# Kernel tuning notes

Measured on AMD Instinct MI355X. Metric: run time of the kernel, lower is better.

The kernel has to match this reference:

```python
import jax, jax.numpy as jnp
import numpy as np

N = 3072
F_IN = 512
H1 = 256
HFC = 64
OUT_DIM = 16
NUM_POOL = 3
P_CUT = 30.0  # ps[0]: percentile threshold on positive attention entries
CC_ITERS = 16  # min-label propagation w/ pointer jumping; reach >= 2^16 hops


def l2norm(x):
    # torch F.normalize(p=2, dim=1)
    return x / jnp.clip(jnp.linalg.norm(x, axis=1, keepdims=True), 1e-12, None)


def gcn(x, adj, W, b):
    # standard Kipf GraphConvolution: adj @ (x @ W) + b
    return adj @ (x @ W) + b


def normalize_adj(adj, k):
    n = adj.shape[0]
    A = adj + k * jnp.eye(n, dtype=adj.dtype)
    D = jnp.sqrt(A.sum(0))
    return A / (D[:, None] * D[None, :])


def edge_score(x, adj, a, W, b):
    h = x @ W + b                               # (n, HFC)
    s1 = h @ a[:HFC]                            # (n,)
    s2 = h @ a[HFC:]
    e = jax.nn.sigmoid(s1[:, None] + s2[None, :])
    att = jnp.where(adj > 0, e, jnp.zeros((), e.dtype))
    att = 0.5 * (att + att.T)
    i = jnp.arange(att.shape[0])
    return att.at[i, i].set(1.0)


def percentile_pos(att, p):
    # np.percentile(att[att>0], p) with linear interpolation, jit-safe
    pos = att > 0
    n_pos = pos.sum()
    s = jnp.sort(jnp.where(pos, att, jnp.inf).ravel())
    idx = (n_pos - 1).astype(att.dtype) * (p / 100.0)
    lo = jnp.floor(idx).astype(jnp.int32)
    hi = jnp.ceil(idx).astype(jnp.int32)
    frac = idx - lo.astype(att.dtype)
    return s[lo] * (1.0 - frac) + s[hi] * frac


def cc_labels(mask):
    # connected components via min-label propagation + pointer jumping.
    # diag of mask is always True (att diag = 1), so every node has a neighbor.
    n = mask.shape[0]
    def step(labels, _):
        neigh = jnp.min(jnp.where(mask, labels[None, :], n), axis=1)
        new = jnp.minimum(labels, neigh)
        new = new[new]  # pointer jumping doubles reach each iter
        return new, None
    labels, _ = jax.lax.scan(step, jnp.arange(n, dtype=jnp.int32), None, length=CC_ITERS)
    return labels


def pool(x, adj, att, p):
    cut = percentile_pos(att, p)
    att = att * (att >= cut).astype(att.dtype)
    labels = jax.lax.stop_gradient(cc_labels(att > 0))
    # fixed-shape membership: cluster id = representative (min) node index, padded to N
    C = jax.nn.one_hot(labels, att.shape[0], dtype=x.dtype).T  # (n_clusters=n, n)
    a2 = C @ adj @ C.T
    a2 = 0.5 * (a2 + a2.T)
    cnt = (att > 0).sum(1).astype(x.dtype)  # >=1 since diag survives the cut
    x2 = C @ ((att / cnt[:, None]) @ x)
    return x2, a2, C


def forward(x, adjC, adj, encW0, encb0, encW, encb, fcW, fcb, aW, decW, decb, decW_out, decb_out):
    adjs = [adj]
    adjCs = [adjC]
    xs, Cs, atts = [], [], []
    # ----- encode -----
    for k in range(NUM_POOL):
        x1 = x
        W, b = (encW0, encb0) if k == 0 else (encW[k - 1], encb[k - 1])
        h = jax.nn.relu(gcn(x, adjCs[-1], W, b))
        x = l2norm(h) if k == 0 else l2norm(h + x1)  # residual added for layer idx > 0
        xs.append(x)
        att = edge_score(x, adjs[-1], aW[k], fcW[k], fcb[k])
        x, adjk, C = pool(x, adjs[-1], att, P_CUT)
        adjCk = normalize_adj(adjk, 1.0)  # pool's adjC output is discarded in the original
        x = l2norm(x)
        adjs.append(adjk)
        adjCs.append(adjCk)
        atts.append(att)
        Cs.append(C)
    x = l2norm(jax.nn.elu(gcn(x, adjCs[-1], encW[NUM_POOL - 1], encb[NUM_POOL - 1])))
    xs.append(x)
    # ----- decode -----
    for k in range(NUM_POOL):
        lev = NUM_POOL - k - 1
        x = Cs[lev].T @ x                       # unpool; C is already binary
        x = jnp.concatenate([x, xs[lev]], axis=1)
        x = l2norm(jax.nn.elu(gcn(x, adjCs[lev], decW[k], decb[k])))
    x = gcn(x, adjCs[0], decW_out, decb_out)
    logp = jax.nn.log_softmax(x, axis=1)
    return logp, jnp.stack(Cs), jnp.stack(atts)


def setup_inputs() -> dict:
    key = jax.random.key(0)
    ks = jax.random.split(key, 12)
    x = jax.random.normal(ks[0], (N, F_IN), jnp.float32)
    u = jax.random.uniform(ks[1], (N, N))
    m = (u < 16.0 / N).astype(jnp.float32)  # avg degree ~16
    adj = jnp.maximum(m, m.T)
    i = jnp.arange(N)
    adj = adj.at[i, i].set(1.0)
    adjC = normalize_adj(adj, 1.0)

    def xav(k, shape):
        fan_in = shape[-2] if len(shape) > 1 else shape[-1]
        return jax.random.normal(k, shape, jnp.float32) * (1.0 / np.sqrt(fan_in))

    return {
        "x": x, "adjC": adjC, "adj": adj,
        "encW0": xav(ks[2], (F_IN, H1)), "encb0": jnp.zeros((H1,), jnp.float32),
        "encW": xav(ks[3], (NUM_POOL, H1, H1)), "encb": jnp.zeros((NUM_POOL, H1), jnp.float32),
        "fcW": xav(ks[4], (NUM_POOL, H1, HFC)), "fcb": jnp.zeros((NUM_POOL, HFC), jnp.float32),
        "aW": xav(ks[5], (NUM_POOL, 2 * HFC)),
        "decW": xav(ks[6], (NUM_POOL, 2 * H1, H1)), "decb": jnp.zeros((NUM_POOL, H1), jnp.float32),
        "decW_out": xav(ks[7], (H1, OUT_DIM)), "decb_out": jnp.zeros((OUT_DIM,), jnp.float32),
    }


def reference(x, adjC, adj, encW0, encb0, encW, encb, fcW, fcb, aW, decW, decb, decW_out, decb_out):
    return forward(x, adjC, adj, encW0, encb0, encW, encb, fcW, fcb, aW, decW, decb, decW_out, decb_out)
```

## Files before the change

### kernel.cpp

```cpp
#include <hip/hip_runtime.h>
#include <math.h>

#define NN 3072
#define FF 256
#define CAPE (1<<18)
#define MAXCH 3200

struct Scal {
  int nnzS, nnz2, nzero, mtot, ncht;
  int lo, hi, rank_rem, below_acc, c_le;
  unsigned prefix, vlo, minabove;
  float frac, cut;
};

__device__ __forceinline__ float sigm(float x){ return 1.0f/(1.0f+expf(-x)); }

__global__ __launch_bounds__(256) void k_count_dense(const float* __restrict__ A, int* __restrict__ rowcnt, float* __restrict__ Drow){
  int i=blockIdx.x, t=threadIdx.x;
  int c=0; float sm=0.f;
  for(int j=t;j<NN;j+=256){ float a=A[(size_t)i*NN+j]; if(a!=0.0f||j==i) c++; sm+=a; }
  __shared__ int s[256]; __shared__ float fs[256];
  s[t]=c; fs[t]=sm; __syncthreads();
  for(int o=128;o;o>>=1){ if(t<o){ s[t]+=s[t+o]; fs[t]+=fs[t+o]; } __syncthreads(); }
  if(t==0){ rowcnt[i]=s[0]; if(Drow) Drow[i]=sqrtf(fs[0]+1.0f); }
}

__global__ __launch_bounds__(1024) void k_scan(const int* __restrict__ cnt, int* __restrict__ rp, int* __restrict__ total){
  int t=threadIdx.x;
  int a0=cnt[t*3+0], a1=cnt[t*3+1], a2=cnt[t*3+2];
  int loc=a0+a1+a2;
  __shared__ int s[1024];
  s[t]=loc; __syncthreads();
  for(int o=1;o<1024;o<<=1){ int v=(t>=o)?s[t-o]:0; __syncthreads(); s[t]+=v; __syncthreads(); }
  int excl=s[t]-loc;
  rp[t*3+0]=excl; rp[t*3+1]=excl+a0; rp[t*3+2]=excl+a0+a1;
  if(t==1023){ rp[NN]=s[t]; *total=s[t]; }
}

__global__ __launch_bounds__(256) void k_fill_dense(const float* __restrict__ A, const float* __restrict__ ACd, const float* __restrict__ D,
    const int* __restrict__ rp, int* __restrict__ rows, int* __restrict__ cols, float* __restrict__ aval, float* __restrict__ acval){
  int i=blockIdx.x, t=threadIdx.x;
  const int CH=NN/256;
  int j0=t*CH; int c=0;
  for(int u=0;u<CH;u++){ int j=j0+u; float a=A[(size_t)i*NN+j]; if(a!=0.0f||j==i) c++; }
  __shared__ int s[256]; s[t]=c; __syncthreads();
  for(int o=1;o<256;o<<=1){ int v=(t>=o)?s[t-o]:0; __syncthreads(); s[t]+=v; __syncthreads(); }
  int pos=rp[i]+s[t]-c;
  float Di = D?D[i]:0.0f;
  for(int u=0;u<CH;u++){ int j=j0+u; float a=A[(size_t)i*NN+j];
    if(a!=0.0f||j==i){
      if(pos<CAPE){
        rows[pos]=i; cols[pos]=j; aval[pos]=a;
        acval[pos]= ACd? ACd[(size_t)i*NN+j] : (a+(j==i?1.0f:0.0f))/(Di*D[j]);
      }
      pos++;
    }
  }
}

__global__ __launch_bounds__(256) void k_gemm(const float* __restrict__ A, const float* __restrict__ B, float* __restrict__ C,
                                              int M, int K, int Nc){
  __shared__ float As[16][68];
  __shared__ float Bs[16][68];
  int tid=threadIdx.x;
  int tx=tid&15, ty=tid>>4;
  int bm=blockIdx.y*64, bn=blockIdx.x*64;
  int lm=tid>>2, lk=(tid&3)*4;
  int kr=tid>>4, nf=(tid&15)*4;
  float acc[4][4]={};
  for(int k0=0;k0<K;k0+=16){
    float4 a4=*(const float4*)(A+(size_t)(bm+lm)*K+k0+lk);
    As[lk+0][lm]=a4.x; As[lk+1][lm]=a4.y; As[lk+2][lm]=a4.z; As[lk+3][lm]=a4.w;
    float4 b4=*(const float4*)(B+(size_t)(k0+kr)*Nc+bn+nf);
    *(float4*)&Bs[kr][nf]=b4;
    __syncthreads();
#pragma unroll
    for(int kk=0;kk<16;kk++){
      float4 av=*(const float4*)&As[kk][ty*4];
      float4 bv=*(const float4*)&Bs[kk][tx*4];
      float am[4]={av.x,av.y,av.z,av.w};
      float bb[4]={bv.x,bv.y,bv.z,bv.w};
#pragma unroll
      for(int i2=0;i2<4;i2++)
#pragma unroll
        for(int j2=0;j2<4;j2++) acc[i2][j2]+=am[i2]*bb[j2];
    }
    __syncthreads();
  }
  for(int i2=0;i2<4;i2++){
    float4 o=make_float4(acc[i2][0],acc[i2][1],acc[i2][2],acc[i2][3]);
    *(float4*)(C+(size_t)(bm+ty*4+i2)*Nc+bn+tx*4)=o;
  }
}

__global__ __launch_bounds__(256) void k_gemm16(const float* __restrict__ X, const float* __restrict__ W, float* __restrict__ T){
  int idx=blockIdx.x*256+threadIdx.x;
  if(idx>=NN*16) return;
  int i=idx>>4, o=idx&15;
  float s=0.f;
  for(int kk=0;kk<FF;kk++) s+=X[(size_t)i*FF+kk]*W[kk*16+o];
  T[idx]=s;
}

__global__ __launch_bounds__(256) void k_spmm_gcn(const int* __restrict__ rp, const int* __restrict__ cols, const float* __restrict__ vals,
    const float* __restrict__ X, const float* __restrict__ bias, const float* __restrict__ resid, float* __restrict__ out, int act){
  int wid=blockIdx.x*4+(threadIdx.x>>6);
  int lane=threadIdx.x&63;
  if(wid>=NN) return;
  int e0=rp[wid], e1=rp[wid+1];
  float4 acc=make_float4(0,0,0,0);
  for(int e=e0;e<e1;e++){
    float v=vals[e]; int c=cols[e];
    float4 xv=*(const float4*)(X+(size_t)c*FF+lane*4);
    acc.x+=v*xv.x; acc.y+=v*xv.y; acc.z+=v*xv.z; acc.w+=v*xv.w;
  }
  float4 bv=*(const float4*)(bias+lane*4);
  acc.x+=bv.x; acc.y+=bv.y; acc.z+=bv.z; acc.w+=bv.w;
  if(act==0){
    acc.x=fmaxf(acc.x,0.f); acc.y=fmaxf(acc.y,0.f); acc.z=fmaxf(acc.z,0.f); acc.w=fmaxf(acc.w,0.f);
  } else {
    acc.x=acc.x>0.f?acc.x:expm1f(acc.x); acc.y=acc.y>0.f?acc.y:expm1f(acc.y);
    acc.z=acc.z>0.f?acc.z:expm1f(acc.z); acc.w=acc.w>0.f?acc.w:expm1f(acc.w);
  }
  if(resid){
    float4 r=*(const float4*)(resid+(size_t)wid*FF+lane*4);
    acc.x+=r.x; acc.y+=r.y; acc.z+=r.z; acc.w+=r.w;
  }
  float ss=acc.x*acc.x+acc.y*acc.y+acc.z*acc.z+acc.w*acc.w;
  for(int o=32;o;o>>=1) ss+=__shfl_xor(ss,o);
  float nrm=fmaxf(sqrtf(ss),1e-12f);
  float4 o4=make_float4(acc.x/nrm,acc.y/nrm,acc.z/nrm,acc.w/nrm);
  *(float4*)(out+(size_t)wid*FF+lane*4)=o4;
}

__global__ __launch_bounds__(256) void k_spmm_plain(const int* __restrict__ rp, const int* __restrict__ cols, const float* __restrict__ vals,
    const float* __restrict__ X, float* __restrict__ out){
  int wid=blockIdx.x*4+(threadIdx.x>>6);
  int lane=threadIdx.x&63;
  if(wid>=NN) return;
  int e0=rp[wid], e1=rp[wid+1];
  float4 acc=make_float4(0,0,0,0);
  for(int e=e0;e<e1;e++){
    if(e>=CAPE) break;
    float v=vals[e]; int c=cols[e];
    float4 xv=*(const float4*)(X+(size_t)c*FF+lane*4);
    acc.x+=v*xv.x; acc.y+=v*xv.y; acc.z+=v*xv.z; acc.w+=v*xv.w;
  }
  *(float4*)(out+(size_t)wid*FF+lane*4)=acc;
}

__global__ __launch_bounds__(64) void k_edge(const float* __restrict__ X, const float* __restrict__ fw, const float* __restrict__ fb,
    const float* __restrict__ av, float* __restrict__ s1, float* __restrict__ s2, Scal* sc){
  int i=blockIdx.x, l=threadIdx.x;
  if(i==0&&l==0) sc->nzero=0;
  __shared__ float xr[FF];
  *(float4*)&xr[l*4]=*(const float4*)(X+(size_t)i*FF+l*4);
  __syncthreads();
  float h=fb[l];
  for(int kk=0;kk<FF;kk++) h+=xr[kk]*fw[kk*64+l];
  float p1=h*av[l], p2=h*av[64+l];
  for(int o=32;o;o>>=1){ p1+=__shfl_xor(p1,o); p2+=__shfl_xor(p2,o); }
  if(l==0){ s1[i]=p1; s2[i]=p2; }
}

__global__ __launch_bounds__(256) void k_att_row(const int* __restrict__ rp, const int* __restrict__ cols,
    const float* __restrict__ s1, const float* __restrict__ s2, float* __restrict__ attD, float* __restrict__ cand, Scal* sc){
  __shared__ float row[NN];
  __shared__ int wred[4];
  int i=blockIdx.x, t=threadIdx.x;
  for(int j=t;j<NN;j+=256) row[j]=0.f;
  __syncthreads();
  int e0=rp[i], e1=rp[i+1];
  float s1i=s1[i], s2i=s2[i];
  int nz=0;
  for(int e=e0+t;e<e1;e+=256){
    int j=cols[e];
    float v=(j==i)?1.0f:0.5f*(sigm(s1i+s2[j])+sigm(s1[j]+s2i));
    row[j]=v;
    if(e<CAPE) cand[e]=v;
    if(!(v>0.f)) nz++;
  }
  for(int o=32;o;o>>=1) nz+=__shfl_xor(nz,o);
  if((t&63)==0) wred[t>>6]=nz;
  __syncthreads();
  if(t==0){ int s=wred[0]+wred[1]+wred[2]+wred[3]; if(s) atomicAdd(&sc->nzero,s); }
  float* orow=attD+(size_t)i*NN;
  for(int j=t*4;j<NN;j+=1024) *(float4*)(orow+j)=*(const float4*)&row[j];
}

__global__ void k_prep(Scal* sc){
  int np=sc->nnzS - sc->nzero;
  float idx=(float)(np-1)*(30.0f/100.0f);
  float fl=floorf(idx), ce=ceilf(idx);
  sc->lo=(int)fl; sc->hi=(int)ce; sc->frac=idx-fl;
  sc->rank_rem=sc->lo;
  sc->below_acc=0;
  sc->minabove=0xFFFFFFFFu;
}

template<int PHASE>
__global__ __launch_bounds__(256) void k_hist(const float* __restrict__ cand, const Scal* __restrict__ sc, unsigned* __restrict__ bins){
  const int NB = (PHASE==0)?16384:256;
  __shared__ unsigned h[NB];
  int t=threadIdx.x;
  for(int b=t;b<NB;b+=256) h[b]=0;
  __syncthreads();
  int n=sc->nnzS; if(n>CAPE) n=CAPE;
  unsigned pref=sc->prefix;
  int stride=gridDim.x*256;
  for(int e=blockIdx.x*256+t; e<n; e+=stride){
    float v=cand[e];
    if(!(v>0.f)) continue;
    unsigned bb=__float_as_uint(v);
    if(PHASE==0) atomicAdd(&h[bb>>16],1u);
    else if(PHASE==1){ if((bb>>16)==pref) atomicAdd(&h[(bb>>8)&0xFFu],1u); }
    else { if((bb>>8)==pref) atomicAdd(&h[bb&0xFFu],1u); }
  }
  __syncthreads();
  for(int b=t;b<NB;b+=256){ unsigned c=h[b]; if(c) atomicAdd(&bins[b],c); }
}

template<int PHASE>
__global__ __launch_bounds__(256) void k_pick(const unsigned* __restrict__ bins, Scal* sc){
  const int NB=(PHASE==0)?16384:256;
  const int PER=NB/256;
  __shared__ int part[256];
  __shared__ int selbin; __shared__ int below_sel;
  int t=threadIdx.x;
  int b0=t*PER;
  int sum=0;
  for(int u=0;u<PER;u++) sum+=(int)bins[b0+u];
  part[t]=sum; __syncthreads();
  for(int o=1;o<256;o<<=1){ int v=(t>=o)?part[t-o]:0; __syncthreads(); part[t]+=v; __syncthreads(); }
  int incl=part[t], excl=incl-sum;
  int r=sc->rank_rem;
  if(r>=excl && r<incl){
    int run=excl;
    for(int u=0;u<PER;u++){
      int c=(int)bins[b0+u];
      if(r<run+c){ selbin=b0+u; below_sel=run; break; }
      run+=c;
    }
  }
  __syncthreads();
  if(t==0){
    sc->rank_rem=r-below_sel;
    sc->below_acc+=below_sel;
    if(PHASE==0) sc->prefix=(unsigned)selbin;
    else if(PHASE==1) sc->prefix=(sc->prefix<<8)|(unsigned)selbin;
    else{
      sc->vlo=(sc->prefix<<8)|(unsigned)selbin;
      sc->c_le=sc->below_acc+(int)bins[selbin];
    }
  }
}

__global__ __launch_bounds__(256) void k_minabove(const float* __restrict__ cand, Scal* sc){
  int n=sc->nnzS; if(n>CAPE) n=CAPE;
  unsigned vlo=sc->vlo;
  int tid=threadIdx.x, lane=tid&63;
  int stride=gridDim.x*256;
  for(int base=blockIdx.x*256; base<n; base+=stride){
    int e=base+tid;
    unsigned b=0xFFFFFFFFu;
    if(e<n){ float v=cand[e]; if(v>0.f){ unsigned bb=__float_as_uint(v); if(bb>vlo) b=bb; } }
    for(int o=32;o;o>>=1){ unsigned ob=__shfl_xor(b,o); b=ob<b?ob:b; }
    if(lane==0&&b!=0xFFFFFFFFu) atomicMin(&sc->minabove,b);
  }
}

__global__ void k_cut(Scal* sc){
  float slo=__uint_as_float(sc->vlo);
  float shi;
  if(sc->hi==sc->lo) shi=slo;
  else if(sc->c_le>sc->hi) shi=slo;
  else shi=__uint_as_float(sc->minabove);
  sc->cut=slo*(1.0f-sc->frac)+shi*sc->frac;
}

__global__ __launch_bounds__(256) void k_pc_count(const int* __restrict__ rp, const float* __restrict__ cand, const Scal* __restrict__ sc,
    int* __restrict__ rowcnt, float* __restrict__ cntf){
  int wid=blockIdx.x*4+(threadIdx.x>>6);
  int lane=threadIdx.x&63;
  if(wid>=NN) return;
  int e0=rp[wid], e1=rp[wid+1];
  float cut=sc->cut;
  int c=0;
  for(int e=e0+lane;e<e1;e+=64){ if(e<CAPE && cand[e]>=cut) c++; }
  for(int o=32;o;o>>=1) c+=__shfl_xor(c,o);
  if(lane==0){ rowcnt[wid]=c; cntf[wid]=(float)c; }
}

__global__ __launch_bounds__(256) void k_pc_fill(const int* __restrict__ rp, const int* __restrict__ cols, const float* __restrict__ cand,
    const Scal* __restrict__ sc, const int* __restrict__ rp2, int* __restrict__ rows2, int* __restrict__ cols2, float* __restrict__ pval,
    const float* __restrict__ cntf){
  int wid=blockIdx.x*4+(threadIdx.x>>6);
  int lane=threadIdx.x&63;
  if(wid>=NN) return;
  int e0=rp[wid], e1=rp[wid+1];
  float cut=sc->cut, cf=cntf[wid];
  int base=rp2[wid];
  for(int eb=e0;eb<e1;eb+=64){
    int e=eb+lane;
    bool p=(e<e1)&&(e<CAPE)&&(cand[e]>=cut);
    unsigned long long m=__ballot(p);
    if(p){
      int pos=base+__popcll(m&((1ull<<lane)-1ull));
      if(pos<CAPE){ rows2[pos]=wid; cols2[pos]=cols[e]; pval[pos]=cand[e]/cf; }
    }
    base+=__popcll(m);
  }
}

__global__ __launch_bounds__(1024) void k_cc(const int* __restrict__ rows2, const int* __restrict__ cols2, Scal* sc,
    int* __restrict__ labk, int* __restrict__ moff_g, int* __restrict__ memb,
    int* __restrict__ choff_g, int* __restrict__ chm0_g, int* __restrict__ chm1_g){
  __shared__ int lab[NN];
  __shared__ int cnt[NN];
  __shared__ int mof[NN];
  __shared__ int s[1024];
  __shared__ int chg;
  int t=threadIdx.x;
  for(int i=t;i<NN;i+=1024){ lab[i]=i; cnt[i]=0; }
  int n2=sc->nnz2; if(n2>CAPE) n2=CAPE;
  __syncthreads();
  for(int it=0;it<16;it++){
    if(t==0) chg=0;
    __syncthreads();
    for(int e=t;e<n2;e+=1024){
      int i=rows2[e], j=cols2[e];
      if(i!=j){
        int li=lab[i], lj=lab[j];
        if(lj<li){ if(atomicMin(&lab[i],lj)>lj) chg=1; }
        else if(li<lj){ if(atomicMin(&lab[j],li)>li) chg=1; }
      }
    }
    __syncthreads();
    int l0=lab[t], l1=lab[t+1024], l2=lab[t+2048];
    int v0=lab[l0], v1=lab[l1], v2=lab[l2];
    __syncthreads();
    if(v0<l0){ lab[t]=v0; chg=1; }
    if(v1<l1){ lab[t+1024]=v1; chg=1; }
    if(v2<l2){ lab[t+2048]=v2; chg=1; }
    __syncthreads();
    if(!chg) break;
    __syncthreads();
  }
  for(int i=t;i<NN;i+=1024){ int l=lab[i]; labk[i]=l; atomicAdd(&cnt[l],1); }
  __syncthreads();
  int a0=cnt[t*3+0], a1=cnt[t*3+1], a2=cnt[t*3+2];
  int loc=a0+a1+a2;
  s[t]=loc; __syncthreads();
  for(int o=1;o<1024;o<<=1){ int v=(t>=o)?s[t-o]:0; __syncthreads(); s[t]+=v; __syncthreads(); }
  int excl=s[t]-loc;
  __syncthreads();
  mof[t*3+0]=excl; mof[t*3+1]=excl+a0; mof[t*3+2]=excl+a0+a1;
  cnt[t*3+0]=excl; cnt[t*3+1]=excl+a0; cnt[t*3+2]=excl+a0+a1;
  moff_g[t*3+0]=excl; moff_g[t*3+1]=excl+a0; moff_g[t*3+2]=excl+a0+a1;
  if(t==1023) moff_g[NN]=s[t];
  __syncthreads();
  int ch0=(a0+63)>>6, ch1=(a1+63)>>6, ch2=(a2+63)>>6;
  int locc=ch0+ch1+ch2;
  s[t]=locc; __syncthreads();
  for(int o=1;o<1024;o<<=1){ int v=(t>=o)?s[t-o]:0; __syncthreads(); s[t]+=v; __syncthreads(); }
  int cexcl=s[t]-locc;
  choff_g[t*3+0]=cexcl; choff_g[t*3+1]=cexcl+ch0; choff_g[t*3+2]=cexcl+ch0+ch1;
  if(t==1023){ choff_g[NN]=s[t]; sc->ncht=s[t]; }
  {
    int bases[3]={cexcl,cexcl+ch0,cexcl+ch0+ch1};
    int cnts[3]={a0,a1,a2};
    int nqs[3]={ch0,ch1,ch2};
    for(int u=0;u<3;u++){
      int m0=mof[t*3+u];
      int me=m0+cnts[u];
      for(int q=0;q<nqs[u];q++){
        int idx=bases[u]+q;
        if(idx<MAXCH){
          chm0_g[idx]=m0+q*64;
          int e2=m0+q*64+64; chm1_g[idx]=e2<me?e2:me;
        }
      }
    }
  }
  __syncthreads();
  int lane=t&63, wv=t>>6;
  for(int b=0;b<3;b++){
    int j=b*1024+t;
    int myl=lab[j];
    int rank_w=0,total=0;
#pragma unroll
    for(int l=0;l<64;l++){
      int lb=__shfl(myl,l);
      if(lb==myl){ total++; if(l<lane) rank_w++; }
    }
    for(int w=0;w<16;w++){
      if(wv==w){
        int base=cnt[myl];
        memb[base+rank_w]=j;
        if(rank_w==0) cnt[myl]=base+total;
      }
      __syncthreads();
    }
  }
}

__global__ __launch_bounds__(256) void k_a2e(const int* __restrict__ rowsA, const int* __restrict__ colsA_, const float* __restrict__ aval,
    const Scal* __restrict__ sc, const int* __restrict__ labk, float* __restrict__ dense){
  int e=blockIdx.x*256+threadIdx.x;
  int n=sc->nnzS; if(n>CAPE) n=CAPE;
  int lane=threadIdx.x&63;
  bool valid=(e<n);
  float a=valid?aval[e]:0.f;
  valid=valid&&(a!=0.f);
  int key=0;
  if(valid) key=labk[rowsA[e]]*NN+labk[colsA_[e]];
  unsigned long long act=__ballot(valid);
  while(act){
    int leader=__ffsll(act)-1;
    int lkey=__shfl(key,leader);
    bool same=valid&&(key==lkey);
    float contrib=same?a:0.f;
    for(int o=32;o;o>>=1) contrib+=__shfl_xor(contrib,o);
    if(lane==leader) atomicAdd(&dense[(size_t)lkey],contrib);
    act&=~__ballot(same);
  }
}

__global__ __launch_bounds__(256) void k_x2p(const float* __restrict__ y, const int* __restrict__ memb,
    const int* __restrict__ chm0, const int* __restrict__ chm1, const Scal* __restrict__ sc, float* __restrict__ partial){
  int b=blockIdx.x;
  if(b>=sc->ncht||b>=MAXCH) return;
  int t=threadIdx.x;
  int m0=chm0[b], m1=chm1[b];
  float acc=0.f;
#pragma unroll 4
  for(int m=m0;m<m1;m++) acc+=y[(size_t)memb[m]*FF+t];
  partial[(size_t)b*FF+t]=acc;
}
__global__ __launch_bounds__(256) void k_x2f(const int* __restrict__ choff, const float* __restrict__ partial, float* __restrict__ out){
  int c=blockIdx.x, t=threadIdx.x;
  int q0=choff[c], q1=choff[c+1];
  float acc=0.f;
  for(int q=q0;q<q1&&q<MAXCH;q++) acc+=partial[(size_t)q*FF+t];
  __shared__ float red[256];
  red[t]=acc*acc; __syncthreads();
  for(int o=128;o;o>>=1){ if(t<o) red[t]+=red[t+o]; __syncthreads(); }
  float nrm=fmaxf(sqrtf(red[0]),1e-12f);
  out[(size_t)c*FF+t]=(q1>q0)?acc/nrm:0.f;
}

__global__ __launch_bounds__(256) void k_gather(const float* __restrict__ X, const int* __restrict__ labs, const float* __restrict__ xsk,
    float* __restrict__ xcat){
  int idx=blockIdx.x*256+threadIdx.x;
  if(idx>=NN*128) return;
  int j=idx>>7, f4=idx&127;
  float4 v;
  if(f4<64) v=*(const float4*)(X+(size_t)labs[j]*FF+f4*4);
  else v=*(const float4*)(xsk+(size_t)j*FF+(size_t)(f4-64)*4);
  *(float4*)(xcat+(size_t)j*512+(size_t)f4*4)=v;
}

__global__ __launch_bounds__(256) void k_final(const int* __restrict__ rp, const int* __restrict__ cols, const float* __restrict__ vals,
    const float* __restrict__ T, const float* __restrict__ bias, float* __restrict__ logp){
  int i=blockIdx.x*256+threadIdx.x;
  if(i>=NN) return;
  float o[16];
#pragma unroll
  for(int f=0;f<16;f++) o[f]=bias[f];
  int e1=rp[i+1];
  for(int e=rp[i];e<e1;e++){
    float v=vals[e]; const float* tr=T+(size_t)cols[e]*16;
#pragma unroll
    for(int f=0;f<16;f++) o[f]+=v*tr[f];
  }
  float m=o[0];
#pragma unroll
  for(int f=1;f<16;f++) m=fmaxf(m,o[f]);
  float ssum=0.f;
#pragma unroll
  for(int f=0;f<16;f++) ssum+=expf(o[f]-m);
  float lse=logf(ssum);
#pragma unroll
  for(int f=0;f<16;f++) logp[(size_t)i*16+f]=o[f]-m-lse;
}

__global__ __launch_bounds__(256) void k_cfill(const int* __restrict__ labsv, float* __restrict__ CsB){
  int idx=blockIdx.x*256+threadIdx.x;
  if(idx>=3*NN) return;
  int l=idx/NN, j=idx-l*NN;
  int c=labsv[l*NN+j];
  CsB[(size_t)l*NN*NN+(size_t)c*NN+j]=1.0f;
}

extern "C" void kernel_launch(void* const* d_in, const int* in_sizes, int n_in,
                              void* d_out, int out_size, void* d_ws, size_t ws_size,
                              hipStream_t stream) {
  (void)in_sizes; (void)n_in; (void)out_size;
  const float* x_in =(const float*)d_in[0];
  const float* adjC =(const float*)d_in[1];
  const float* adj  =(const float*)d_in[2];
  const float* encW0=(const float*)d_in[3];
  const float* encb0=(const float*)d_in[4];
  const float* encW =(const float*)d_in[5];
  const float* encb =(const float*)d_in[6];
  const float* fcW  =(const float*)d_in[7];
  const float* fcb  =(const float*)d_in[8];
  const float* aW   =(const float*)d_in[9];
  const float* decW =(const float*)d_in[10];
  const float* decb =(const float*)d_in[11];
  const float* decWo=(const float*)d_in[12];
  const float* decbo=(const float*)d_in[13];
  float* out=(float*)d_out;

  float* logp=out;
  float* CsB = out + (size_t)NN*16;
  float* attB= CsB + 3ull*NN*NN;
  float* slot1 = CsB + (size_t)NN*NN;
  float* xs[4]; for(int i=0;i<4;i++) xs[i]=slot1+(size_t)i*NN*FF;
  float* xcur=slot1+(size_t)4*NN*FF;
  float* ybuf=slot1+(size_t)5*NN*FF;
  float* tbuf=slot1+(size_t)6*NN*FF;
  float* slot2 = CsB + 2ull*NN*NN;
  float* xcat=slot2;
  float* t16 = xcat + (size_t)NN*512;

  char* w=(char*)d_ws; size_t off=0;
  auto alc=[&](size_t b)->void*{ off=(off+255)&~(size_t)255; void* r=w+off; off+=b; return r; };
  Scal* sc=(Scal*)alc(sizeof(Scal));
  int* rowcnt=(int*)alc((size_t)NN*4);
  int* rp[4]; for(int i=0;i<4;i++) rp[i]=(int*)alc((size_t)(NN+1)*4);
  int* rp2=(int*)alc((size_t)(NN+1)*4);
  int* colsA[4]; float* acv[4];
  for(int i=0;i<4;i++){ colsA[i]=(int*)alc((size_t)CAPE*4); acv[i]=(float*)alc((size_t)CAPE*4); }
  float* avalS=(float*)alc((size_t)CAPE*4);
  int* rowsA=(int*)alc((size_t)CAPE*4);
  float* cand=(float*)alc((size_t)CAPE*4);
  int* rows2=(int*)alc((size_t)CAPE*4);
  int* cols2=(int*)alc((size_t)CAPE*4);
  float* pval=(float*)alc((size_t)CAPE*4);
  unsigned* bins=(unsigned*)alc((size_t)16384*4);
  int* labsv=(int*)alc((size_t)3*NN*4);
  int* moff=(int*)alc((size_t)(NN+1)*4);
  int* memb=(int*)alc((size_t)NN*4);
  int* choff=(int*)alc((size_t)(NN+1)*4);
  int* chm0=(int*)alc((size_t)MAXCH*4);
  int* chm1=(int*)alc((size_t)MAXCH*4);
  float* partial=(float*)alc((size_t)MAXCH*FF*4);
  float* cntf=(float*)alc((size_t)NN*4);
  float* s1=(float*)alc((size_t)NN*4);
  float* s2v=(float*)alc((size_t)NN*4);
  float* Dv=(float*)alc((size_t)NN*4);
  float* dense;
  size_t denseB=(size_t)NN*NN*4;
  if(ws_size>=off+denseB+4096) dense=(float*)alc(denseB);
  else dense=CsB;

  auto build_csr=[&](const float* Ad, const float* ACd, const float* Dp, int lvl){
    k_count_dense<<<NN,256,0,stream>>>(Ad,rowcnt,Dv);
    k_scan<<<1,1024,0,stream>>>(rowcnt,rp[lvl],&sc->nnzS);
    k_fill_dense<<<NN,256,0,stream>>>(Ad,ACd,Dp,rp[lvl],rowsA,colsA[lvl],avalS,acv[lvl]);
  };

  build_csr(adj,adjC,nullptr,0);

  for(int k=0;k<3;k++){
    const float* xin=(k==0)?x_in:xcur;
    const float* Wk=(k==0)?encW0:(encW+(size_t)(k-1)*FF*FF);
    const float* bk=(k==0)?encb0:(encb+(size_t)(k-1)*FF);
    int K=(k==0)?512:FF;
    k_gemm<<<dim3(FF/64,NN/64),256,0,stream>>>(xin,Wk,tbuf,NN,K,FF);
    k_spmm_gcn<<<NN/4,256,0,stream>>>(rp[k],colsA[k],acv[k],tbuf,bk,(k==0)?nullptr:xcur,xs[k],0);

    k_edge<<<NN,64,0,stream>>>(xs[k],fcW+(size_t)k*FF*64,fcb+(size_t)k*64,aW+(size_t)k*128,s1,s2v,sc);
    k_att_row<<<NN,256,0,stream>>>(rp[k],colsA[k],s1,s2v,attB+(size_t)k*NN*NN,cand,sc);

    k_prep<<<1,1,0,stream>>>(sc);
    hipMemsetAsync(bins,0,(size_t)16384*4,stream);
    k_hist<0><<<64,256,0,stream>>>(cand,sc,bins);
    k_pick<0><<<1,256,0,stream>>>(bins,sc);
    hipMemsetAsync(bins,0,(size_t)256*4,stream);
    k_hist<1><<<64,256,0,stream>>>(cand,sc,bins);
    k_pick<1><<<1,256,0,stream>>>(bins,sc);
    hipMemsetAsync(bins,0,(size_t)256*4,stream);
    k_hist<2><<<64,256,0,stream>>>(cand,sc,bins);
    k_pick<2><<<1,256,0,stream>>>(bins,sc);
    k_minabove<<<256,256,0,stream>>>(cand,sc);
    k_cut<<<1,1,0,stream>>>(sc);

    k_pc_count<<<NN/4,256,0,stream>>>(rp[k],cand,sc,rowcnt,cntf);
    k_scan<<<1,1024,0,stream>>>(rowcnt,rp2,&sc->nnz2);
    k_pc_fill<<<NN/4,256,0,stream>>>(rp[k],colsA[k],cand,sc,rp2,rows2,cols2,pval,cntf);

    k_cc<<<1,1024,0,stream>>>(rows2,cols2,sc,labsv+(size_t)k*NN,moff,memb,choff,chm0,chm1);

    hipMemsetAsync(dense,0,denseB,stream);
    k_a2e<<<CAPE/256,256,0,stream>>>(rowsA,colsA[k],avalS,sc,labsv+(size_t)k*NN,dense);

    k_spmm_plain<<<NN/4,256,0,stream>>>(rp2,cols2,pval,xs[k],ybuf);
    k_x2p<<<MAXCH,256,0,stream>>>(ybuf,memb,chm0,chm1,sc,partial);
    k_x2f<<<NN,256,0,stream>>>(choff,partial,xcur);

    build_csr(dense,nullptr,Dv,k+1);
  }

  k_gemm<<<dim3(FF/64,NN/64),256,0,stream>>>(xcur,encW+(size_t)2*FF*FF,tbuf,NN,FF,FF);
  k_spmm_gcn<<<NN/4,256,0,stream>>>(rp[3],colsA[3],acv[3],tbuf,encb+(size_t)2*FF,nullptr,xs[3],1);

  float* xd=xs[3];
  float* outsb[3]={xcur,ybuf,xcur};
  for(int k=0;k<3;k++){
    int lev=2-k;
    k_gather<<<(NN*128)/256,256,0,stream>>>(xd,labsv+(size_t)lev*NN,xs[lev],xcat);
    k_gemm<<<dim3(FF/64,NN/64),256,0,stream>>>(xcat,decW+(size_t)k*512*FF,tbuf,NN,512,FF);
    k_spmm_gcn<<<NN/4,256,0,stream>>>(rp[lev],colsA[lev],acv[lev],tbuf,decb+(size_t)k*FF,nullptr,outsb[k],1);
    xd=outsb[k];
  }

  k_gemm16<<<(NN*16)/256,256,0,stream>>>(xd,decWo,t16);
  k_final<<<(NN+255)/256,256,0,stream>>>(rp[0],colsA[0],acv[0],t16,decbo,logp);

  hipMemsetAsync(CsB,0,3ull*NN*NN*4,stream);
  k_cfill<<<(3*NN+255)/256,256,0,stream>>>(labsv,CsB);
}
```

Measured before the change: 915.7 us.

## Cut launches: fuse prep into pick, atomic row allocation, single-pass cluster-matrix fill

Result: slower. 993.0 us (+8.4%).

```diff
diff --git a/kernel.cpp b/kernel.cpp
--- a/kernel.cpp
+++ b/kernel.cpp
@@ -133,12 +133,12 @@
   *(float4*)(out+(size_t)wid*FF+lane*4)=o4;
 }
 
-__global__ __launch_bounds__(256) void k_spmm_plain(const int* __restrict__ rp, const int* __restrict__ cols, const float* __restrict__ vals,
-    const float* __restrict__ X, float* __restrict__ out){
+__global__ __launch_bounds__(256) void k_spmm_plain(const int* __restrict__ rs, const int* __restrict__ rl,
+    const int* __restrict__ cols, const float* __restrict__ vals, const float* __restrict__ X, float* __restrict__ out){
   int wid=blockIdx.x*4+(threadIdx.x>>6);
   int lane=threadIdx.x&63;
   if(wid>=NN) return;
-  int e0=rp[wid], e1=rp[wid+1];
+  int e0=rs[wid], e1=e0+rl[wid];
   float4 acc=make_float4(0,0,0,0);
   for(int e=e0;e<e1;e++){
     if(e>=CAPE) break;
@@ -186,16 +186,6 @@
   if(t==0){ int s=wred[0]+wred[1]+wred[2]+wred[3]; if(s) atomicAdd(&sc->nzero,s); }
   float* orow=attD+(size_t)i*NN;
   for(int j=t*4;j<NN;j+=1024) *(float4*)(orow+j)=*(const float4*)&row[j];
-}
-
-__global__ void k_prep(Scal* sc){
-  int np=sc->nnzS - sc->nzero;
-  float idx=(float)(np-1)*(30.0f/100.0f);
-  float fl=floorf(idx), ce=ceilf(idx);
-  sc->lo=(int)fl; sc->hi=(int)ce; sc->frac=idx-fl;
-  sc->rank_rem=sc->lo;
-  sc->below_acc=0;
-  sc->minabove=0xFFFFFFFFu;
 }
 
 template<int PHASE>
@@ -221,19 +211,32 @@
 }
 
 template<int PHASE>
-__global__ __launch_bounds__(256) void k_pick(const unsigned* __restrict__ bins, Scal* sc){
+__global__ __launch_bounds__(256) void k_pick(unsigned* __restrict__ bins, Scal* sc){
   const int NB=(PHASE==0)?16384:256;
   const int PER=NB/256;
   __shared__ int part[256];
-  __shared__ int selbin; __shared__ int below_sel;
+  __shared__ int selbin; __shared__ int below_sel; __shared__ int sh_r;
   int t=threadIdx.x;
+  if(t==0){
+    int r;
+    if(PHASE==0){
+      int np=sc->nnzS - sc->nzero;
+      float idx=(float)(np-1)*(30.0f/100.0f);
+      float fl=floorf(idx), ce=ceilf(idx);
+      sc->lo=(int)fl; sc->hi=(int)ce; sc->frac=idx-fl;
+      sc->below_acc=0; sc->minabove=0xFFFFFFFFu;
+      r=(int)fl;
+    } else r=sc->rank_rem;
+    sh_r=r;
+  }
+  __syncthreads();
+  int r=sh_r;
   int b0=t*PER;
   int sum=0;
   for(int u=0;u<PER;u++) sum+=(int)bins[b0+u];
   part[t]=sum; __syncthreads();
   for(int o=1;o<256;o<<=1){ int v=(t>=o)?part[t-o]:0; __syncthreads(); part[t]+=v; __syncthreads(); }
   int incl=part[t], excl=incl-sum;
-  int r=sc->rank_rem;
   if(r>=excl && r<incl){
     int run=excl;
     for(int u=0;u<PER;u++){
@@ -252,6 +255,10 @@
       sc->vlo=(sc->prefix<<8)|(unsigned)selbin;
       sc->c_le=sc->below_acc+(int)bins[selbin];
     }
+  }
+  if(PHASE<2){
+    __syncthreads();
+    if(t<256) bins[t]=0;
   }
 }
 
@@ -276,10 +283,12 @@
   else if(sc->c_le>sc->hi) shi=slo;
   else shi=__uint_as_float(sc->minabove);
   sc->cut=slo*(1.0f-sc->frac)+shi*sc->frac;
-}
-
-__global__ __launch_bounds__(256) void k_pc_count(const int* __restrict__ rp, const float* __restrict__ cand, const Scal* __restrict__ sc,
-    int* __restrict__ rowcnt, float* __restrict__ cntf){
+  sc->nnz2=0;
+}
+
+__global__ __launch_bounds__(256) void k_pc(const int* __restrict__ rp, const int* __restrict__ cols,
+    const float* __restrict__ cand, Scal* sc, int* __restrict__ rs2, int* __restrict__ rl2,
+    int* __restrict__ rows2, int* __restrict__ cols2, float* __restrict__ pval){
   int wid=blockIdx.x*4+(threadIdx.x>>6);
   int lane=threadIdx.x&63;
   if(wid>=NN) return;
@@ -288,18 +297,13 @@
   int c=0;
   for(int e=e0+lane;e<e1;e+=64){ if(e<CAPE && cand[e]>=cut) c++; }
   for(int o=32;o;o>>=1) c+=__shfl_xor(c,o);
-  if(lane==0){ rowcnt[wid]=c; cntf[wid]=(float)c; }
-}
-
-__global__ __launch_bounds__(256) void k_pc_fill(const int* __restrict__ rp, const int* __restrict__ cols, const float* __restrict__ cand,
-    const Scal* __restrict__ sc, const int* __restrict__ rp2, int* __restrict__ rows2, int* __restrict__ cols2, float* __restrict__ pval,
-    const float* __restrict__ cntf){
-  int wid=blockIdx.x*4+(threadIdx.x>>6);
-  int lane=threadIdx.x&63;
-  if(wid>=NN) return;
-  int e0=rp[wid], e1=rp[wid+1];
-  float cut=sc->cut, cf=cntf[wid];
-  int base=rp2[wid];
+  int base=0;
+  if(lane==0){
+    base=atomicAdd(&sc->nnz2,c);
+    rs2[wid]=base; rl2[wid]=c;
+  }
+  base=__shfl(base,0);
+  float cf=(float)c;
   for(int eb=e0;eb<e1;eb+=64){
     int e=eb+lane;
     bool p=(e<e1)&&(e<CAPE)&&(cand[e]>=cut);
@@ -484,12 +488,21 @@
   for(int f=0;f<16;f++) logp[(size_t)i*16+f]=o[f]-m-lse;
 }
 
-__global__ __launch_bounds__(256) void k_cfill(const int* __restrict__ labsv, float* __restrict__ CsB){
+__global__ __launch_bounds__(256) void k_cs_full(const int* __restrict__ labsv, float* __restrict__ CsB){
   int idx=blockIdx.x*256+threadIdx.x;
-  if(idx>=3*NN) return;
-  int l=idx/NN, j=idx-l*NN;
-  int c=labsv[l*NN+j];
-  CsB[(size_t)l*NN*NN+(size_t)c*NN+j]=1.0f;
+  const int ROW4=NN/4;
+  int l=idx/(NN*ROW4);
+  int rem=idx-l*(NN*ROW4);
+  int c=rem/ROW4;
+  int j4=(rem-c*ROW4)*4;
+  const int* lb=labsv+(size_t)l*NN+j4;
+  int4 lv=*(const int4*)lb;
+  float4 o;
+  o.x=(lv.x==c)?1.0f:0.0f;
+  o.y=(lv.y==c)?1.0f:0.0f;
+  o.z=(lv.z==c)?1.0f:0.0f;
+  o.w=(lv.w==c)?1.0f:0.0f;
+  *(float4*)(CsB+(size_t)idx*4)=o;
 }
 
 extern "C" void kernel_launch(void* const* d_in, const int* in_sizes, int n_in,
@@ -529,12 +542,13 @@
   Scal* sc=(Scal*)alc(sizeof(Scal));
   int* rowcnt=(int*)alc((size_t)NN*4);
   int* rp[4]; for(int i=0;i<4;i++) rp[i]=(int*)alc((size_t)(NN+1)*4);
-  int* rp2=(int*)alc((size_t)(NN+1)*4);
   int* colsA[4]; float* acv[4];
   for(int i=0;i<4;i++){ colsA[i]=(int*)alc((size_t)CAPE*4); acv[i]=(float*)alc((size_t)CAPE*4); }
   float* avalS=(float*)alc((size_t)CAPE*4);
   int* rowsA=(int*)alc((size_t)CAPE*4);
   float* cand=(float*)alc((size_t)CAPE*4);
+  int* rs2=(int*)alc((size_t)NN*4);
+  int* rl2=(int*)alc((size_t)NN*4);
   int* rows2=(int*)alc((size_t)CAPE*4);
   int* cols2=(int*)alc((size_t)CAPE*4);
   float* pval=(float*)alc((size_t)CAPE*4);
@@ -546,7 +560,6 @@
   int* chm0=(int*)alc((size_t)MAXCH*4);
   int* chm1=(int*)alc((size_t)MAXCH*4);
   float* partial=(float*)alc((size_t)MAXCH*FF*4);
-  float* cntf=(float*)alc((size_t)NN*4);
   float* s1=(float*)alc((size_t)NN*4);
   float* s2v=(float*)alc((size_t)NN*4);
   float* Dv=(float*)alc((size_t)NN*4);
@@ -574,29 +587,24 @@
     k_edge<<<NN,64,0,stream>>>(xs[k],fcW+(size_t)k*FF*64,fcb+(size_t)k*64,aW+(size_t)k*128,s1,s2v,sc);
     k_att_row<<<NN,256,0,stream>>>(rp[k],colsA[k],s1,s2v,attB+(size_t)k*NN*NN,cand,sc);
 
-    k_prep<<<1,1,0,stream>>>(sc);
     hipMemsetAsync(bins,0,(size_t)16384*4,stream);
     k_hist<0><<<64,256,0,stream>>>(cand,sc,bins);
     k_pick<0><<<1,256,0,stream>>>(bins,sc);
-    hipMemsetAsync(bins,0,(size_t)256*4,stream);
     k_hist<1><<<64,256,0,stream>>>(cand,sc,bins);
     k_pick<1><<<1,256,0,stream>>>(bins,sc);
-    hipMemsetAsync(bins,0,(size_t)256*4,stream);
     k_hist<2><<<64,256,0,stream>>>(cand,sc,bins);
     k_pick<2><<<1,256,0,stream>>>(bins,sc);
     k_minabove<<<256,256,0,stream>>>(cand,sc);
     k_cut<<<1,1,0,stream>>>(sc);
 
-    k_pc_count<<<NN/4,256,0,stream>>>(rp[k],cand,sc,rowcnt,cntf);
-    k_scan<<<1,1024,0,stream>>>(rowcnt,rp2,&sc->nnz2);
-    k_pc_fill<<<NN/4,256,0,stream>>>(rp[k],colsA[k],cand,sc,rp2,rows2,cols2,pval,cntf);
+    k_pc<<<NN/4,256,0,stream>>>(rp[k],colsA[k],cand,sc,rs2,rl2,rows2,cols2,pval);
 
     k_cc<<<1,1024,0,stream>>>(rows2,cols2,sc,labsv+(size_t)k*NN,moff,memb,choff,chm0,chm1);
 
     hipMemsetAsync(dense,0,denseB,stream);
     k_a2e<<<CAPE/256,256,0,stream>>>(rowsA,colsA[k],avalS,sc,labsv+(size_t)k*NN,dense);
 
-    k_spmm_plain<<<NN/4,256,0,stream>>>(rp2,cols2,pval,xs[k],ybuf);
+    k_spmm_plain<<<NN/4,256,0,stream>>>(rs2,rl2,cols2,pval,xs[k],ybuf);
     k_x2p<<<MAXCH,256,0,stream>>>(ybuf,memb,chm0,chm1,sc,partial);
     k_x2f<<<NN,256,0,stream>>>(choff,partial,xcur);
 
@@ -619,6 +627,5 @@
   k_gemm16<<<(NN*16)/256,256,0,stream>>>(xd,decWo,t16);
   k_final<<<(NN+255)/256,256,0,stream>>>(rp[0],colsA[0],acv[0],t16,decbo,logp);
 
-  hipMemsetAsync(CsB,0,3ull*NN*NN*4,stream);
-  k_cfill<<<(3*NN+255)/256,256,0,stream>>>(labsv,CsB);
-}
+  k_cs_full<<<(3*NN*(NN/4))/256,256,0,stream>>>(labsv,CsB);
+}
```
